# Kernel optimization log

Measured on AMD Instinct MI355X. Metric: run time of the kernel, lower is better.

The kernel has to match this reference:

```python
import jax, jax.numpy as jnp
import numpy as np


def _patch_desc(x, patch_size):
    # x: (n, c, h, w). Replicate-pad by patch_size//2 and gather all
    # patch_size*patch_size shifted views -> (n, c*p*p, h*w) descriptors.
    n, c, h, w = x.shape
    step = patch_size // 2
    y = jnp.pad(x, ((0, 0), (0, 0), (step, step), (step, step)), mode='edge')
    feats = [y[:, :, i:i + h, j:j + w]
             for i in range(patch_size) for j in range(patch_size)]
    d = jnp.stack(feats, axis=2)            # (n, c, p*p, h, w)
    return d.reshape(n, c * patch_size * patch_size, h * w)


def setup_inputs() -> dict:
    key = jax.random.key(0)
    k1, k2 = jax.random.split(key)
    n, c, h, w = 4, 16, 64, 64
    s = jax.random.normal(k1, (n, c, h, w), dtype=jnp.float32)
    t = jax.random.normal(k2, (n, c, h, w), dtype=jnp.float32)
    return {"s": s, "t": t, "patch_size": 3}


def reference(s, t, patch_size):
    n, c, h, w = s.shape
    q = _patch_desc(s, patch_size)          # (n, d, hw) source queries
    p = _patch_desc(t, patch_size)          # (n, d, hw) target points
    # Squared-L2 nearest neighbor per source patch (exact version of FLANN kNN)
    qn = jnp.sum(q * q, axis=1)             # (n, hw)
    pn = jnp.sum(p * p, axis=1)             # (n, hw)
    cross = jnp.einsum('ndi,ndj->nij', q, p)  # (n, hw_q, hw_t)
    d2 = qn[:, :, None] - 2.0 * cross + pn[:, None, :]
    idx = jnp.argmin(d2, axis=2)            # (n, hw) flat target index
    nnd = jnp.min(d2, axis=2)               # (n, hw) squared distance
    idy = idx // w
    idx_x = idx % w
    nnf = jnp.stack([idy.reshape(n, h, w), idx_x.reshape(n, h, w)], axis=1)
    nnd = nnd.reshape(n, 1, h, w)
    return nnf.astype(jnp.int32), nnd
```

## Files before the change

### kernel.cpp

```cpp
#include <hip/hip_runtime.h>


#define N_  4
#define C_  16
#define H_  64
#define W_  64
#define HW_ 4096
#define KK_ 18
#define SPLITS_M 8
#define KKSTRIDE 512

#define SPLITS_V 4
#define TILES_PER_SPLIT_V 4

typedef _Float16 f16;
typedef _Float16 f16x8 __attribute__((ext_vector_type(8)));
typedef float    f32x4 __attribute__((ext_vector_type(4)));
typedef float    f32x16 __attribute__((ext_vector_type(16)));

__device__ __forceinline__ int iclamp(int v, int lo, int hi) {
    return v < lo ? lo : (v > hi ? hi : v);
}

__device__ __forceinline__ void async_ld16(const void* g, void* l) {
    __builtin_amdgcn_global_load_lds(
        (const __attribute__((address_space(1))) unsigned int*)g,
        (__attribute__((address_space(3))) unsigned int*)l, 16, 0, 0);
}

__global__ __launch_bounds__(256)
void build_desc_norms_kernel(const float* __restrict__ s,
                             const float* __restrict__ t,
                             f16* __restrict__ Qh, f16* __restrict__ Ql,
                             f16* __restrict__ Ph, f16* __restrict__ Pl,
                             float* __restrict__ pn,
                             float* __restrict__ qn) {
    const int y0  = blockIdx.x;
    const int n   = blockIdx.y;
    const int src = blockIdx.z;
    const float* img = (src ? s : t) + n * (C_ * HW_);
    f16* Dh = src ? Qh : Ph;
    f16* Dl = src ? Ql : Pl;
    float* nrm = src ? qn : pn;

    __shared__ float imgS[3][C_][W_];
    __shared__ float nS[4][W_];
    const int tid = threadIdx.x;
    #pragma unroll
    for (int k = 0; k < 12; ++k) {
        const int idx = tid + k * 256;
        const int x = idx & 63, c = (idx >> 6) & 15, r = idx >> 10;
        const int gy = iclamp(y0 + r - 1, 0, H_ - 1);
        imgS[r][c][x] = img[c * HW_ + gy * W_ + x];
    }
    __syncthreads();

    const int q = tid >> 6, x = tid & 63;
    const int pix = y0 * W_ + x;
    float nacc = 0.f;
    #pragma unroll
    for (int u = 0; u < 5; ++u) {
        const int kk = q * 5 + u;
        if (kk < KK_) {
            f16x8 hv, lv;
            const int d  = kk >> 1;
            const int c0 = (kk & 1) * 8;
            const int dy = (d * 11) >> 5;
            const int dx = d - dy * 3;
            const int xs = iclamp(x + dx - 1, 0, W_ - 1);
            #pragma unroll
            for (int cc = 0; cc < 8; ++cc) {
                const float v = imgS[dy][c0 + cc][xs];
                const f16 h = (f16)v;
                hv[cc] = h;
                lv[cc] = (f16)(v - (float)h);
                nacc += v * v;
            }
            const size_t off = ((size_t)(n * KK_ + kk) * HW_ + pix) * 8;
            *(f16x8*)&Dh[off] = hv;
            *(f16x8*)&Dl[off] = lv;
        }
    }
    nS[q][x] = nacc;
    __syncthreads();
    if (tid < W_)
        nrm[n * HW_ + pix] = nS[0][tid] + nS[1][tid] + nS[2][tid] + nS[3][tid];
}

__global__ __launch_bounds__(256, 2)
void mfma_nn_kernel(const f16* __restrict__ Qh, const f16* __restrict__ Ql,
                    const f16* __restrict__ Ph, const f16* __restrict__ Pl,
                    const float* __restrict__ pn_g,
                    unsigned long long* __restrict__ partial) {
    const int bid   = blockIdx.x;
    const int split = bid & 7;
    const int n     = (bid >> 3) & 3;
    const int iblk  = bid >> 5;
    const int tid  = threadIdx.x;
    const int wave = tid >> 6, lane = tid & 63;
    const int col  = lane & 31;
    const int half = lane >> 5;
    const int irow0 = iblk * 128 + wave * 32;

    __shared__ f16 B0[16 * KKSTRIDE];
    __shared__ f16 B1[16 * KKSTRIDE];
    __shared__ f16 B2[16 * KKSTRIDE];
    __shared__ float pnS[512];

    f16x8 Ah[9], Al[9];
    #pragma unroll
    for (int c = 0; c < 9; ++c) {
        const size_t off = ((size_t)(n * KK_ + 2 * c + half) * HW_ +
                            irow0 + col) * 8;
        Ah[c] = *(const f16x8*)(Qh + off);
        Al[c] = *(const f16x8*)(Ql + off);
    }

    const int jsplit0 = split * 512;
    pnS[tid]       = pn_g[n * HW_ + jsplit0 + tid];
    pnS[tid + 256] = pn_g[n * HW_ + jsplit0 + tid + 256];

    const f16* p8h = Ph + ((size_t)(n * KK_ + 16 + half) * HW_ + jsplit0) * 8;
    const f16* p8l = Pl + ((size_t)(n * KK_ + 16 + half) * HW_ + jsplit0) * 8;

    float    bd[16];
    unsigned bj[16];
    #pragma unroll
    for (int r = 0; r < 16; ++r) { bd[r] = -3.0e38f; bj[r] = 0u; }

    const int kk0 = wave * 4;
    const f16* sbase = half ? Pl : Ph;

    #define STAGE(BUF, T)                                                     \
        {   _Pragma("unroll")                                                 \
            for (int u = 0; u < 4; ++u) {                                     \
                const int kk = kk0 + u;                                       \
                const f16* g = sbase + ((size_t)(n * KK_ + kk) * HW_ +        \
                                        jsplit0 + (T) * 32 + col) * 8;        \
                async_ld16(g, (void*)&BUF[kk * KKSTRIDE + lane * 8]);         \
            }                                                                 \
        }

    #define PHASE(WN, SBUF, ST, DOST, CBUF, CT)                               \
        {   asm volatile("s_waitcnt vmcnt(" #WN ")" ::: "memory");            \
            asm volatile("s_barrier" ::: "memory");                           \
            const int j8 = (CT) * 32 + col;                                   \
            const f16x8 b8h = *(const f16x8*)(p8h + (size_t)j8 * 8);          \
            const f16x8 b8l = *(const f16x8*)(p8l + (size_t)j8 * 8);          \
            if (DOST) STAGE(SBUF, ST);                                        \
            const float pnv = -0.5f * pnS[j8];                                \
            f32x16 Cf;                                                        \
            _Pragma("unroll")                                                 \
            for (int r = 0; r < 16; ++r) Cf[r] = pnv;                         \
            __builtin_amdgcn_s_setprio(1);                                    \
            _Pragma("unroll")                                                 \
            for (int c = 0; c < 8; ++c) {                                     \
                const int kb = (2 * c + half) * KKSTRIDE + col * 8;           \
                const f16x8 bh = *(const f16x8*)&CBUF[kb];                    \
                const f16x8 bl = *(const f16x8*)&CBUF[kb + 256];              \
                Cf = __builtin_amdgcn_mfma_f32_32x32x16_f16(                  \
                    Ah[c], bh, Cf, 0, 0, 0);                                  \
                Cf = __builtin_amdgcn_mfma_f32_32x32x16_f16(                  \
                    Al[c], bh, Cf, 0, 0, 0);                                  \
                Cf = __builtin_amdgcn_mfma_f32_32x32x16_f16(                  \
                    Ah[c], bl, Cf, 0, 0, 0);                                  \
            }                                                                 \
            Cf = __builtin_amdgcn_mfma_f32_32x32x16_f16(                      \
                Ah[8], b8h, Cf, 0, 0, 0);                                     \
            Cf = __builtin_amdgcn_mfma_f32_32x32x16_f16(                      \
                Al[8], b8h, Cf, 0, 0, 0);                                     \
            Cf = __builtin_amdgcn_mfma_f32_32x32x16_f16(                      \
                Ah[8], b8l, Cf, 0, 0, 0);                                     \
            __builtin_amdgcn_s_setprio(0);                                    \
            _Pragma("unroll")                                                 \
            for (int r = 0; r < 16; ++r)                                      \
                if (Cf[r] > bd[r]) { bd[r] = Cf[r]; bj[r] = (unsigned)j8; }   \
        }

    STAGE(B0, 0)
    STAGE(B1, 1)
    __syncthreads();

    for (int g = 0; g < 4; ++g) {
        const int t = g * 3;
        PHASE(4, B2, t + 2, true,  B0, t)
        PHASE(4, B0, t + 3, true,  B1, t + 1)
        PHASE(4, B1, t + 4, true,  B2, t + 2)
    }
    PHASE(4, B2, 14, true,  B0, 12)
    PHASE(4, B0, 15, true,  B1, 13)
    PHASE(4, B1, 0,  false, B2, 14)
    PHASE(0, B0, 0,  false, B0, 15)
    #undef STAGE
    #undef PHASE

    #pragma unroll
    for (int r = 0; r < 16; ++r) {
        float    d = bd[r];
        unsigned j = (unsigned)jsplit0 + bj[r];
        #pragma unroll
        for (int off = 1; off < 32; off <<= 1) {
            const float    od = __shfl_xor(d, off, 64);
            const unsigned oj = __shfl_xor(j, off, 64);
            const bool take = (od > d) || (od == d && oj < j);
            d = take ? od : d;
            j = take ? oj : j;
        }
        if (col == 0) {
            const int i = irow0 + (r & 3) + 8 * (r >> 2) + 4 * half;
            partial[(size_t)(split * N_ + n) * HW_ + i] =
                ((unsigned long long)j << 32) |
                (unsigned long long)__float_as_uint(-2.f * d);
        }
    }
}

__global__ __launch_bounds__(256)
void finalize_mfma_kernel(const unsigned long long* __restrict__ partial,
                          const float* __restrict__ qn_g,
                          float* __restrict__ out) {
    const int id  = blockIdx.x * 256 + threadIdx.x;
    const int n   = id >> 12;
    const int pix = id & 4095;
    float    bd = 3.0e38f;
    unsigned bj = 0u;
    #pragma unroll
    for (int sp = 0; sp < SPLITS_M; ++sp) {
        const unsigned long long v = partial[(size_t)(sp * N_ + n) * HW_ + pix];
        const float    d = __uint_as_float((unsigned)(v & 0xffffffffull));
        const unsigned j = (unsigned)(v >> 32);
        const bool take = (d < bd) || (d == bd && j < bj);
        bd = take ? d : bd;
        bj = take ? j : bj;
    }
    out[n * 2 * HW_ + pix]            = (float)(bj >> 6);
    out[n * 2 * HW_ + HW_ + pix]      = (float)(bj & 63);
    out[N_ * 2 * HW_ + n * HW_ + pix] = bd + qn_g[n * HW_ + pix];
}

__global__ __launch_bounds__(256)
void prep_norms_kernel(const float* __restrict__ s,
                       const float* __restrict__ t,
                       float* __restrict__ pn,
                       float* __restrict__ qn) {
    const int gid   = blockIdx.x * 256 + threadIdx.x;
    const int which = gid >> 14;
    const int id    = gid & 16383;
    const int n     = id >> 12;
    const int pix   = id & 4095;
    const int y = pix >> 6, x = pix & 63;
    const float* base = (which ? s : t) + n * (C_ * HW_);
    float acc = 0.f;
    for (int c = 0; c < C_; ++c) {
        const float* bc = base + c * HW_;
        #pragma unroll
        for (int dy = 0; dy < 3; ++dy) {
            const float* br = bc + iclamp(y + dy - 1, 0, H_ - 1) * W_;
            #pragma unroll
            for (int dx = 0; dx < 3; ++dx) {
                float v = br[iclamp(x + dx - 1, 0, W_ - 1)];
                acc += v * v;
            }
        }
    }
    (which ? qn : pn)[id] = acc;
}

__global__ __launch_bounds__(256)
void patchmatch_main_kernel(const float* __restrict__ s,
                            const float* __restrict__ t,
                            const float* __restrict__ pn_g,
                            const float* __restrict__ qn_g,
                            unsigned long long* __restrict__ partial) {
    const int yq    = blockIdx.x;
    const int n     = blockIdx.y;
    const int split = blockIdx.z;
    const int tid  = threadIdx.x;
    const int tx   = tid & 15;
    const int ty   = tid >> 4;
    const int i0   = ty * 4;
    const int jrow = tx >> 2;
    const int jx0  = (tx & 3) * 16;

    __shared__ float qS[C_][3][68];
    __shared__ float tS[C_][6][68];
    __shared__ float qnS[W_];

    const float* sb = s + n * (C_ * HW_);
    const float* tb = t + n * (C_ * HW_);

    #pragma unroll
    for (int k = 0; k < 3; ++k) {
        const int id = tid + k * 256;
        const int sg = id & 15;
        const int c  = (id >> 4) & 15;
        const int r  = id >> 8;
        const int gr = iclamp(yq + r - 1, 0, H_ - 1);
        const float4 v = *(const float4*)&sb[c * HW_ + gr * W_ + sg * 4];
        float* dst = &qS[c][r][1 + sg * 4];
        dst[0] = v.x; dst[1] = v.y; dst[2] = v.z; dst[3] = v.w;
    }
    if (tid < 48) {
        const int c  = tid & 15;
        const int r  = tid >> 4;
        const int gr = iclamp(yq + r - 1, 0, H_ - 1);
        qS[c][r][0]  = sb[c * HW_ + gr * W_];
        qS[c][r][65] = sb[c * HW_ + gr * W_ + 63];
    }
    if (tid < W_) qnS[tid] = qn_g[n * HW_ + yq * W_ + tid];

    unsigned long long best[4] = {~0ull, ~0ull, ~0ull, ~0ull};

    for (int ytl = 0; ytl < TILES_PER_SPLIT_V; ++ytl) {
        const int yt = split * TILES_PER_SPLIT_V + ytl;
        __syncthreads();
        #pragma unroll
        for (int k = 0; k < 6; ++k) {
            const int id = tid + k * 256;
            const int sg = id & 15;
            const int c  = (id >> 4) & 15;
            const int r  = id >> 8;
            const int gr = iclamp(4 * yt + r - 1, 0, H_ - 1);
            const float4 v = *(const float4*)&tb[c * HW_ + gr * W_ + sg * 4];
            float* dst = &tS[c][r][1 + sg * 4];
            dst[0] = v.x; dst[1] = v.y; dst[2] = v.z; dst[3] = v.w;
        }
        if (tid < 96) {
            const int c  = tid & 15;
            const int r  = tid >> 4;
            const int gr = iclamp(4 * yt + r - 1, 0, H_ - 1);
            tS[c][r][0]  = tb[c * HW_ + gr * W_];
            tS[c][r][65] = tb[c * HW_ + gr * W_ + 63];
        }
        __syncthreads();

        float acc[4][16];
        #pragma unroll
        for (int a = 0; a < 4; ++a)
            #pragma unroll
            for (int b = 0; b < 16; ++b) acc[a][b] = 0.f;

        for (int c = 0; c < C_; ++c) {
            #pragma unroll
            for (int dy = 0; dy < 3; ++dy) {
                float qv[6], tv[18];
                *(float4*)&qv[0] = *(const float4*)&qS[c][dy][i0];
                *(float2*)&qv[4] = *(const float2*)&qS[c][dy][i0 + 4];
                const float* trow = &tS[c][jrow + dy][jx0];
                *(float4*)&tv[0]  = *(const float4*)&trow[0];
                *(float4*)&tv[4]  = *(const float4*)&trow[4];
                *(float4*)&tv[8]  = *(const float4*)&trow[8];
                *(float4*)&tv[12] = *(const float4*)&trow[12];
                *(float2*)&tv[16] = *(const float2*)&trow[16];
                #pragma unroll
                for (int dx = 0; dx < 3; ++dx)
                    #pragma unroll
                    for (int a = 0; a < 4; ++a)
                        #pragma unroll
                        for (int b = 0; b < 16; ++b)
                            acc[a][b] += qv[a + dx] * tv[b + dx];
            }
        }

        const int jbase = yt * 256 + jrow * W_ + jx0;
        float pnv[16];
        const float* png = &pn_g[n * HW_ + jbase];
        *(float4*)&pnv[0]  = *(const float4*)&png[0];
        *(float4*)&pnv[4]  = *(const float4*)&png[4];
        *(float4*)&pnv[8]  = *(const float4*)&png[8];
        *(float4*)&pnv[12] = *(const float4*)&png[12];
        #pragma unroll
        for (int a = 0; a < 4; ++a) {
            const float qn = qnS[i0 + a];
            #pragma unroll
            for (int b = 0; b < 16; ++b) {
                const float d2 = qn + pnv[b] - 2.f * acc[a][b];
                unsigned long long cand =
                    ((unsigned long long)__float_as_uint(d2) << 32) |
                    (unsigned)(jbase + b);
                best[a] = cand < best[a] ? cand : best[a];
            }
        }
    }

    #pragma unroll
    for (int a = 0; a < 4; ++a) {
        unsigned long long v = best[a];
        #pragma unroll
        for (int mm = 8; mm >= 1; mm >>= 1) {
            unsigned long long o = __shfl_xor(v, mm, 64);
            v = o < v ? o : v;
        }
        best[a] = v;
    }
    if (tx == 0) {
        #pragma unroll
        for (int a = 0; a < 4; ++a)
            partial[((split * N_ + n) * HW_) + yq * W_ + i0 + a] = best[a];
    }
}

__global__ __launch_bounds__(256)
void finalize_kernel(const unsigned long long* __restrict__ partial,
                     float* __restrict__ out) {
    const int id  = blockIdx.x * 256 + threadIdx.x;
    const int n   = id >> 12;
    const int pix = id & 4095;
    unsigned long long best = ~0ull;
    #pragma unroll
    for (int sp = 0; sp < SPLITS_V; ++sp) {
        unsigned long long v = partial[(sp * N_ + n) * HW_ + pix];
        best = v < best ? v : best;
    }
    const unsigned j = (unsigned)(best & 0xffffffffu);
    const float d2 = __uint_as_float((unsigned)(best >> 32));
    out[n * 2 * HW_ + pix]            = (float)(j >> 6);
    out[n * 2 * HW_ + HW_ + pix]      = (float)(j & 63);
    out[N_ * 2 * HW_ + n * HW_ + pix] = d2;
}

__global__ __launch_bounds__(256)
void patchmatch_mono_kernel(const float* __restrict__ s,
                            const float* __restrict__ t,
                            float* __restrict__ out) {
    const int yq  = blockIdx.x;
    const int n   = blockIdx.y;
    const int tid = threadIdx.x;
    const int tx  = tid & 15;
    const int ty  = tid >> 4;
    const int i0  = ty * 4;
    const int jrow = tx >> 3;
    const int jx0  = (tx & 7) * 8;

    __shared__ float qS[C_][3][68];
    __shared__ float tS[C_][4][68];
    __shared__ float pnS[HW_];
    __shared__ float qnS[W_];

    const float* sb = s + n * (C_ * HW_);
    const float* tb = t + n * (C_ * HW_);

    for (int jj = tid; jj < HW_; jj += 256) {
        const int y = jj >> 6, x = jj & 63;
        float acc = 0.f;
        for (int c = 0; c < C_; ++c) {
            const float* tc = tb + c * HW_;
            #pragma unroll
            for (int dy = 0; dy < 3; ++dy) {
                const float* tr = tc + iclamp(y + dy - 1, 0, H_ - 1) * W_;
                #pragma unroll
                for (int dx = 0; dx < 3; ++dx) {
                    float v = tr[iclamp(x + dx - 1, 0, W_ - 1)];
                    acc += v * v;
                }
            }
        }
        pnS[jj] = acc;
    }
    for (int idx = tid; idx < C_ * 3 * 66; idx += 256) {
        const int c   = idx / (3 * 66);
        const int rem = idx - c * (3 * 66);
        const int rr  = rem / 66;
        const int xi  = rem - rr * 66;
        qS[c][rr][xi] = sb[c * HW_ + iclamp(yq + rr - 1, 0, H_ - 1) * W_ +
                           iclamp(xi - 1, 0, W_ - 1)];
    }
    __syncthreads();
    if (tid < W_) {
        float acc = 0.f;
        for (int c = 0; c < C_; ++c)
            #pragma unroll
            for (int dy = 0; dy < 3; ++dy)
                #pragma unroll
                for (int dx = 0; dx < 3; ++dx) {
                    float v = qS[c][dy][tid + dx];
                    acc += v * v;
                }
        qnS[tid] = acc;
    }

    unsigned long long best[4] = {~0ull, ~0ull, ~0ull, ~0ull};
    for (int yt = 0; yt < 32; ++yt) {
        __syncthreads();
        for (int idx = tid; idx < C_ * 4 * 66; idx += 256) {
            const int c   = idx / (4 * 66);
            const int rem = idx - c * (4 * 66);
            const int rr  = rem / 66;
            const int xi  = rem - rr * 66;
            tS[c][rr][xi] = tb[c * HW_ + iclamp(2 * yt + rr - 1, 0, H_ - 1) * W_ +
                               iclamp(xi - 1, 0, W_ - 1)];
        }
        __syncthreads();

        float acc[4][8];
        #pragma unroll
        for (int a = 0; a < 4; ++a)
            #pragma unroll
            for (int b = 0; b < 8; ++b) acc[a][b] = 0.f;

        for (int c = 0; c < C_; ++c) {
            #pragma unroll
            for (int dy = 0; dy < 3; ++dy) {
                float qv[8], tv[12];
                *(float4*)&qv[0] = *(const float4*)&qS[c][dy][i0];
                *(float4*)&qv[4] = *(const float4*)&qS[c][dy][i0 + 4];
                const float* trow = &tS[c][jrow + dy][jx0];
                *(float4*)&tv[0] = *(const float4*)&trow[0];
                *(float4*)&tv[4] = *(const float4*)&trow[4];
                *(float4*)&tv[8] = *(const float4*)&trow[8];
                #pragma unroll
                for (int dx = 0; dx < 3; ++dx)
                    #pragma unroll
                    for (int a = 0; a < 4; ++a)
                        #pragma unroll
                        for (int b = 0; b < 8; ++b)
                            acc[a][b] += qv[a + dx] * tv[b + dx];
            }
        }
        const int rbase = (2 * yt + jrow) * W_ + jx0;
        #pragma unroll
        for (int a = 0; a < 4; ++a) {
            const float qn = qnS[i0 + a];
            #pragma unroll
            for (int b = 0; b < 8; ++b) {
                const int j = rbase + b;
                const float d2 = qn + pnS[j] - 2.f * acc[a][b];
                unsigned long long cand =
                    ((unsigned long long)__float_as_uint(d2) << 32) | (unsigned)j;
                best[a] = cand < best[a] ? cand : best[a];
            }
        }
    }
    #pragma unroll
    for (int a = 0; a < 4; ++a) {
        unsigned long long v = best[a];
        #pragma unroll
        for (int mm = 8; mm >= 1; mm >>= 1) {
            unsigned long long o = __shfl_xor(v, mm, 64);
            v = o < v ? o : v;
        }
        best[a] = v;
    }
    if (tx == 0) {
        #pragma unroll
        for (int a = 0; a < 4; ++a) {
            const int x = i0 + a;
            const unsigned j = (unsigned)(best[a] & 0xffffffffu);
            const float d2 = __uint_as_float((unsigned)(best[a] >> 32));
            const int pix = yq * W_ + x;
            out[n * 2 * HW_ + pix]            = (float)(j >> 6);
            out[n * 2 * HW_ + HW_ + pix]      = (float)(j & 63);
            out[N_ * 2 * HW_ + n * HW_ + pix] = d2;
        }
    }
}

extern "C" void kernel_launch(void* const* d_in, const int* in_sizes, int n_in,
                              void* d_out, int out_size, void* d_ws, size_t ws_size,
                              hipStream_t stream) {
    const float* s = (const float*)d_in[0];
    const float* t = (const float*)d_in[1];
    float* out = (float*)d_out;

    const size_t norm_b  = (size_t)N_ * HW_ * 4;
    const size_t part_b  = (size_t)SPLITS_M * N_ * HW_ * 8;
    const size_t desc_b  = (size_t)N_ * HW_ * KK_ * 8 * 2;
    const size_t need_m  = 2 * norm_b + part_b + 4 * desc_b;

    if (ws_size >= need_m) {
        char* w = (char*)d_ws;
        float* pn = (float*)w;                       w += norm_b;
        float* qn = (float*)w;                       w += norm_b;
        unsigned long long* partial = (unsigned long long*)w; w += part_b;
        f16* Qh = (f16*)w;  w += desc_b;
        f16* Ql = (f16*)w;  w += desc_b;
        f16* Ph = (f16*)w;  w += desc_b;
        f16* Pl = (f16*)w;

        build_desc_norms_kernel<<<dim3(64, N_, 2), 256, 0, stream>>>(
            s, t, Qh, Ql, Ph, Pl, pn, qn);
        mfma_nn_kernel<<<1024, 256, 0, stream>>>(Qh, Ql, Ph, Pl, pn, partial);
        finalize_mfma_kernel<<<64, 256, 0, stream>>>(partial, qn, out);
        return;
    }

    const size_t need_v = 2 * norm_b + (size_t)SPLITS_V * N_ * HW_ * 8;
    if (ws_size >= need_v) {
        float* pn = (float*)d_ws;
        float* qn = pn + N_ * HW_;
        unsigned long long* partial =
            (unsigned long long*)((char*)d_ws + 2 * norm_b);
        prep_norms_kernel<<<128, 256, 0, stream>>>(s, t, pn, qn);
        dim3 grid(H_, N_, SPLITS_V);
        patchmatch_main_kernel<<<grid, 256, 0, stream>>>(s, t, pn, qn, partial);
        finalize_kernel<<<64, 256, 0, stream>>>(partial, out);
        return;
    }

    dim3 grid(H_, N_);
    patchmatch_mono_kernel<<<grid, 256, 0, stream>>>(s, t, out);
}
```

Baseline: 134.7 us.

## Stage all 18 K-slices in LDS with double buffering instead of triple

The last two K-slices of the target tile were read straight from global memory in each phase; now all 18 slices go to LDS, with load work split 5/5/4/4 across waves. The triple-buffered ring with a partial vmcnt wait becomes a double buffer with a full vmcnt(0) wait and barrier per tile. This removes per-phase global loads on the MFMA critical path but shortens prefetch lookahead, so load latency may be exposed more. LDS use changes from 3x16 to 2x18 slices.

```diff
diff --git a/kernel.cpp b/kernel.cpp
--- a/kernel.cpp
+++ b/kernel.cpp
@@ -102,9 +102,8 @@
     const int half = lane >> 5;
     const int irow0 = iblk * 128 + wave * 32;
 
-    __shared__ f16 B0[16 * KKSTRIDE];
-    __shared__ f16 B1[16 * KKSTRIDE];
-    __shared__ f16 B2[16 * KKSTRIDE];
+    __shared__ f16 B0[KK_ * KKSTRIDE];
+    __shared__ f16 B1[KK_ * KKSTRIDE];
     __shared__ float pnS[512];
 
     f16x8 Ah[9], Al[9];
@@ -118,46 +117,46 @@
 
     const int jsplit0 = split * 512;
     pnS[tid]       = pn_g[n * HW_ + jsplit0 + tid];
-    pnS[tid + 256] = pn_g[n * HW_ + jsplit0 + tid + 256];
-
-    const f16* p8h = Ph + ((size_t)(n * KK_ + 16 + half) * HW_ + jsplit0) * 8;
-    const f16* p8l = Pl + ((size_t)(n * KK_ + 16 + half) * HW_ + jsplit0) * 8;
+    if (tid < 256) pnS[tid + 256] = pn_g[n * HW_ + jsplit0 + tid + 256];
 
     float    bd[16];
     unsigned bj[16];
     #pragma unroll
     for (int r = 0; r < 16; ++r) { bd[r] = -3.0e38f; bj[r] = 0u; }
 
-    const int kk0 = wave * 4;
+    const int nst = (wave < 2) ? 5 : 4;
+    const int kk0 = (wave < 2) ? wave * 5 : 10 + (wave - 2) * 4;
     const f16* sbase = half ? Pl : Ph;
 
     #define STAGE(BUF, T)                                                     \
         {   _Pragma("unroll")                                                 \
-            for (int u = 0; u < 4; ++u) {                                     \
-                const int kk = kk0 + u;                                       \
-                const f16* g = sbase + ((size_t)(n * KK_ + kk) * HW_ +        \
-                                        jsplit0 + (T) * 32 + col) * 8;        \
-                async_ld16(g, (void*)&BUF[kk * KKSTRIDE + lane * 8]);         \
+            for (int u = 0; u < 5; ++u) {                                     \
+                if (u < nst) {                                                \
+                    const int kk = kk0 + u;                                   \
+                    const f16* g = sbase + ((size_t)(n * KK_ + kk) * HW_ +    \
+                                            jsplit0 + (T) * 32 + col) * 8;    \
+                    async_ld16(g, (void*)&BUF[kk * KKSTRIDE + lane * 8]);     \
+                }                                                             \
             }                                                                 \
         }
 
-    #define PHASE(WN, SBUF, ST, DOST, CBUF, CT)                               \
-        {   asm volatile("s_waitcnt vmcnt(" #WN ")" ::: "memory");            \
+    #define BAR()                                                             \
+        {   asm volatile("s_waitcnt vmcnt(0)" ::: "memory");                  \
             asm volatile("s_barrier" ::: "memory");                           \
-            const int j8 = (CT) * 32 + col;                                   \
-            const f16x8 b8h = *(const f16x8*)(p8h + (size_t)j8 * 8);          \
-            const f16x8 b8l = *(const f16x8*)(p8l + (size_t)j8 * 8);          \
-            if (DOST) STAGE(SBUF, ST);                                        \
-            const float pnv = -0.5f * pnS[j8];                                \
+        }
+
+    #define COMPUTE(BUF, T)                                                   \
+        {   const int jloc = (T) * 32 + col;                                  \
+            const float pnv = -0.5f * pnS[jloc];                              \
             f32x16 Cf;                                                        \
             _Pragma("unroll")                                                 \
             for (int r = 0; r < 16; ++r) Cf[r] = pnv;                         \
             __builtin_amdgcn_s_setprio(1);                                    \
             _Pragma("unroll")                                                 \
-            for (int c = 0; c < 8; ++c) {                                     \
+            for (int c = 0; c < 9; ++c) {                                     \
                 const int kb = (2 * c + half) * KKSTRIDE + col * 8;           \
-                const f16x8 bh = *(const f16x8*)&CBUF[kb];                    \
-                const f16x8 bl = *(const f16x8*)&CBUF[kb + 256];              \
+                const f16x8 bh = *(const f16x8*)&BUF[kb];                     \
+                const f16x8 bl = *(const f16x8*)&BUF[kb + 256];               \
                 Cf = __builtin_amdgcn_mfma_f32_32x32x16_f16(                  \
                     Ah[c], bh, Cf, 0, 0, 0);                                  \
                 Cf = __builtin_amdgcn_mfma_f32_32x32x16_f16(                  \
@@ -165,34 +164,26 @@
                 Cf = __builtin_amdgcn_mfma_f32_32x32x16_f16(                  \
                     Ah[c], bl, Cf, 0, 0, 0);                                  \
             }                                                                 \
-            Cf = __builtin_amdgcn_mfma_f32_32x32x16_f16(                      \
-                Ah[8], b8h, Cf, 0, 0, 0);                                     \
-            Cf = __builtin_amdgcn_mfma_f32_32x32x16_f16(                      \
-                Al[8], b8h, Cf, 0, 0, 0);                                     \
-            Cf = __builtin_amdgcn_mfma_f32_32x32x16_f16(                      \
-                Ah[8], b8l, Cf, 0, 0, 0);                                     \
             __builtin_amdgcn_s_setprio(0);                                    \
             _Pragma("unroll")                                                 \
             for (int r = 0; r < 16; ++r)                                      \
-                if (Cf[r] > bd[r]) { bd[r] = Cf[r]; bj[r] = (unsigned)j8; }   \
+                if (Cf[r] > bd[r]) { bd[r] = Cf[r]; bj[r] = (unsigned)jloc; } \
         }
 
     STAGE(B0, 0)
-    STAGE(B1, 1)
+    asm volatile("s_waitcnt vmcnt(0)" ::: "memory");
     __syncthreads();
 
-    for (int g = 0; g < 4; ++g) {
-        const int t = g * 3;
-        PHASE(4, B2, t + 2, true,  B0, t)
-        PHASE(4, B0, t + 3, true,  B1, t + 1)
-        PHASE(4, B1, t + 4, true,  B2, t + 2)
-    }
-    PHASE(4, B2, 14, true,  B0, 12)
-    PHASE(4, B0, 15, true,  B1, 13)
-    PHASE(4, B1, 0,  false, B2, 14)
-    PHASE(0, B0, 0,  false, B0, 15)
+    STAGE(B1, 1)  COMPUTE(B0, 0)
+    for (int g = 0; g < 7; ++g) {
+        const int t2 = g * 2;
+        BAR()  STAGE(B0, t2 + 2)  COMPUTE(B1, t2 + 1)
+        BAR()  STAGE(B1, t2 + 3)  COMPUTE(B0, t2 + 2)
+    }
+    BAR()  COMPUTE(B1, 15)
     #undef STAGE
-    #undef PHASE
+    #undef BAR
+    #undef COMPUTE
 
     #pragma unroll
     for (int r = 0; r < 16; ++r) {
```

After: 133.5 us. No clear change (-0.9%).
